# Performance work log

Measured on AMD Instinct MI355X. Metric: run time of the kernel, lower is better.

The kernel has to match this reference:

```python
import jax, jax.numpy as jnp
import numpy as np

N_NODES = 50000
NFEAT, NHID, NSSF, NCLASS = 512, 512, 256, 64
N_EDGES = 1600000
SP_RATE = 0.5
EPS = 1e-6


def spmm(src, dst, vals, m):
    # sparse [N,N] @ dense [N,F]: gather rows by src, scale, scatter-add to dst rows
    return jax.ops.segment_sum(m[src] * vals[:, None], dst, num_segments=N_NODES)


def setup_inputs() -> dict:
    key = jax.random.key(0)
    ks = jax.random.split(key, 12)
    stdv1 = 1.0 / np.sqrt(NFEAT)
    stdv2 = 1.0 / np.sqrt(NHID)
    inp = {
        "x": jax.random.normal(ks[0], (N_NODES, NFEAT), jnp.float32),
        "src": jax.random.randint(ks[1], (N_EDGES,), 0, N_NODES, jnp.int32),
        "dst": jax.random.randint(ks[2], (N_EDGES,), 0, N_NODES, jnp.int32),
        "vals": jax.random.uniform(ks[3], (N_EDGES,), jnp.float32),
        "W1": jax.random.uniform(ks[4], (NFEAT, NHID), jnp.float32, -stdv1, stdv1),
        "b1": jax.random.uniform(ks[5], (NHID,), jnp.float32, -stdv1, stdv1),
        "W2": jax.random.uniform(ks[6], (NHID, NHID), jnp.float32, -stdv2, stdv2),
        "b2": jax.random.uniform(ks[7], (NHID,), jnp.float32, -stdv2, stdv2),
        "W3": jax.random.uniform(ks[8], (NHID, NSSF), jnp.float32, -stdv2, stdv2),
        "b3": jax.random.uniform(ks[9], (NSSF,), jnp.float32, -stdv2, stdv2),
        "ssf": jax.random.normal(ks[10], (NSSF, NCLASS), jnp.float32) * 0.1,
        "sigma": jax.random.normal(ks[11], (), jnp.float32),
    }
    return inp


def reference(x, src, dst, vals, W1, b1, W2, b2, W3, b3, ssf, sigma):
    # 3 GCN layers: spmm(adj, x @ W + b)
    h = spmm(src, dst, vals, x @ W1 + b1)
    h = jax.nn.relu(h)
    h = spmm(src, dst, vals, h @ W2 + b2)
    h = jax.nn.relu(h)
    h = spmm(src, dst, vals, h @ W3 + b3)  # [N, NSSF]

    # sparsify subspace filter by magnitude threshold (static index)
    flat = jnp.abs(ssf).reshape(-1)
    filter_idx = round(NSSF * NCLASS * SP_RATE)
    threshold = jnp.sort(flat)[filter_idx]
    ssf_sp = jnp.where(jnp.abs(ssf) >= threshold, ssf, 0.0)

    out = h @ ssf_sp  # [N, NCLASS]

    # negative euclidean distance to each filter column: cdist(h, ssf_sp.T)
    sq = (jnp.sum(h * h, axis=1)[:, None]
          - 2.0 * out
          + jnp.sum(ssf_sp * ssf_sp, axis=0)[None, :])
    spatial_dist = -jnp.sqrt(jnp.maximum(sq, 1e-12))

    # cosine similarity of each row of h with each filter column
    hn = jnp.maximum(jnp.linalg.norm(h, axis=1), EPS)          # [N]
    cn = jnp.maximum(jnp.linalg.norm(ssf_sp, axis=0), EPS)     # [NCLASS]
    spatial_similarity = out / (hn[:, None] * cn[None, :])

    spatial_loss = 0.5 * (jax.nn.log_softmax(spatial_dist, axis=1)
                          + jax.nn.log_softmax(spatial_similarity, axis=1))
    return (out, ssf_sp, h, spatial_loss, sigma)
```

## Files before the change

kernel.cpp:

```cpp
#include <hip/hip_runtime.h>
#include <hip/hip_bf16.h>
#include <cstddef>

#define NN 50000
#define NE 1600000
#define NFEAT 512
#define NHID 512
#define NSSF 256
#define NCLASS 64
#define KTH 8193

typedef unsigned short u16;
typedef unsigned int u32;
typedef u16 u16x8 __attribute__((ext_vector_type(8)));
typedef u16 u16x4 __attribute__((ext_vector_type(4)));
typedef short bf16x8 __attribute__((ext_vector_type(8)));
typedef float f32x4 __attribute__((ext_vector_type(4)));

__device__ __forceinline__ float bf2f(u16 u) {
  union { unsigned u; float f; } c; c.u = ((unsigned)u) << 16; return c.f;
}
__device__ __forceinline__ u16 f2bf(float f) {
  __hip_bfloat16 b = __float2bfloat16(f);
  union { __hip_bfloat16 b; u16 u; } c; c.b = b; return c.u;
}

__device__ __forceinline__ void async_load16(const void* g, void* l) {
  __builtin_amdgcn_global_load_lds(
      (const __attribute__((address_space(1))) unsigned int*)g,
      (__attribute__((address_space(3))) unsigned int*)l, 16, 0, 0);
}

__global__ void k_hist(const int* __restrict__ dst, int* __restrict__ cnt) {
  int i = blockIdx.x * blockDim.x + threadIdx.x;
  int stride = gridDim.x * blockDim.x;
  for (; i < NE; i += stride) atomicAdd(&cnt[dst[i]], 1);
}

#define SCAN_B 196
__global__ void k_blksum(const int* __restrict__ cnt, int* __restrict__ bsum) {
  __shared__ int red[256];
  int b = blockIdx.x, t = threadIdx.x;
  int i = b * 256 + t;
  red[t] = (i < NN) ? cnt[i] : 0;
  __syncthreads();
  for (int s = 128; s > 0; s >>= 1) { if (t < s) red[t] += red[t + s]; __syncthreads(); }
  if (t == 0) bsum[b] = red[0];
}

__global__ void k_scanb(const int* __restrict__ bsum, int* __restrict__ boff,
                        int* __restrict__ rp) {
  __shared__ int buf[256];
  int t = threadIdx.x;
  int x = (t < SCAN_B) ? bsum[t] : 0;
  buf[t] = x;
  __syncthreads();
  for (int off = 1; off < 256; off <<= 1) {
    int y = (t >= off) ? buf[t - off] : 0;
    __syncthreads();
    buf[t] += y;
    __syncthreads();
  }
  if (t < SCAN_B) boff[t] = buf[t] - x;
  if (t == 0) rp[0] = 0;
}

__global__ void k_scanf(const int* __restrict__ cnt, const int* __restrict__ boff,
                        int* __restrict__ rp, int* __restrict__ fill) {
  __shared__ int buf[256];
  int b = blockIdx.x, t = threadIdx.x;
  int i = b * 256 + t;
  int x = (i < NN) ? cnt[i] : 0;
  buf[t] = x;
  __syncthreads();
  for (int off = 1; off < 256; off <<= 1) {
    int y = (t >= off) ? buf[t - off] : 0;
    __syncthreads();
    buf[t] += y;
    __syncthreads();
  }
  if (i < NN) {
    int incl = boff[b] + buf[t];
    rp[i + 1] = incl;
    fill[i] = incl - x;
  }
}

__global__ void k_scatter(const int* __restrict__ src, const int* __restrict__ dst,
                          const float* __restrict__ vals, int* __restrict__ fill,
                          u32* __restrict__ em) {
  int i = blockIdx.x * blockDim.x + threadIdx.x;
  int stride = gridDim.x * blockDim.x;
  for (; i < NE; i += stride) {
    int p = atomicAdd(&fill[dst[i]], 1);
    em[p] = (u32)src[i] | ((u32)f2bf(vals[i]) << 16);
  }
}

__global__ void k_cvt_bf16(const float* __restrict__ x, u16* __restrict__ xb, int n4) {
  int i = blockIdx.x * blockDim.x + threadIdx.x;
  if (i < n4) {
    float4 v = *(const float4*)(x + (size_t)i * 4);
    u16x4 o;
    o[0] = f2bf(v.x); o[1] = f2bf(v.y); o[2] = f2bf(v.z); o[3] = f2bf(v.w);
    *(u16x4*)(xb + (size_t)i * 4) = o;
  }
}

__global__ void k_wt(const float* __restrict__ W, u16* __restrict__ Wt, int K, int N) {
  int idx = blockIdx.x * blockDim.x + threadIdx.x;
  if (idx < N * K) {
    int n = idx / K, k = idx % K;
    Wt[idx] = f2bf(W[(size_t)k * N + n]);
  }
}

__global__ __launch_bounds__(256, 2) void k_gemm_mfma(
    const u16* __restrict__ A, const u16* __restrict__ Bt,
    const float* __restrict__ bias, u16* __restrict__ C,
    int M, int K, int N)
{
  __shared__ __align__(16) u16 As[128 * 32];
  __shared__ __align__(16) u16 Bs[128 * 32];
  int tid = threadIdx.x;
  int bm = blockIdx.y * 128;
  int bn = blockIdx.x * 128;
  int wave = tid >> 6, lane = tid & 63;

  int lrow = lane >> 2, lcol = (lane & 3) * 8;
  int arow0 = wave * 32 + lrow;
  int arow1 = wave * 32 + 16 + lrow;
  int garow0 = bm + arow0; if (garow0 >= M) garow0 = M - 1;
  int garow1 = bm + arow1; if (garow1 >= M) garow1 = M - 1;
  const u16* Ap0 = A + (size_t)garow0 * K + lcol;
  const u16* Ap1 = A + (size_t)garow1 * K + lcol;
  const u16* Bp0 = Bt + (size_t)(bn + arow0) * K + lcol;
  const u16* Bp1 = Bt + (size_t)(bn + arow1) * K + lcol;
  u16* lA0 = &As[(wave * 32) * 32];
  u16* lA1 = &As[(wave * 32 + 16) * 32];
  u16* lB0 = &Bs[(wave * 32) * 32];
  u16* lB1 = &Bs[(wave * 32 + 16) * 32];

  int wm = (wave >> 1) * 64, wn = (wave & 1) * 64;
  int m16 = lane & 15, quad = lane >> 4;

  f32x4 zz = {0.f, 0.f, 0.f, 0.f};
  f32x4 acc[4][4];
#pragma unroll
  for (int i = 0; i < 4; i++)
#pragma unroll
    for (int j = 0; j < 4; j++) acc[i][j] = zz;

  for (int k0 = 0; k0 < K; k0 += 32) {
    async_load16(Ap0 + k0, lA0);
    async_load16(Ap1 + k0, lA1);
    async_load16(Bp0 + k0, lB0);
    async_load16(Bp1 + k0, lB1);
    __syncthreads();

    bf16x8 af[4], bw[4];
#pragma unroll
    for (int i = 0; i < 4; i++)
      af[i] = *(const bf16x8*)&As[(wm + i * 16 + m16) * 32 + quad * 8];
#pragma unroll
    for (int j = 0; j < 4; j++)
      bw[j] = *(const bf16x8*)&Bs[(wn + j * 16 + m16) * 32 + quad * 8];
#pragma unroll
    for (int i = 0; i < 4; i++)
#pragma unroll
      for (int j = 0; j < 4; j++)
        acc[i][j] = __builtin_amdgcn_mfma_f32_16x16x32_bf16(af[i], bw[j], acc[i][j], 0, 0, 0);
    __syncthreads();
  }

#pragma unroll
  for (int j = 0; j < 4; j++) {
    int col = bn + wn + j * 16 + m16;
    float bv = bias[col];
#pragma unroll
    for (int i = 0; i < 4; i++) {
      int rbase = bm + wm + i * 16 + quad * 4;
#pragma unroll
      for (int r = 0; r < 4; r++) {
        int row = rbase + r;
        if (row < M) C[(size_t)row * N + col] = f2bf(acc[i][j][r] + bv);
      }
    }
  }
}

__global__ __launch_bounds__(256) void k_spmm512(
    const int* __restrict__ rp, const u32* __restrict__ em,
    const u16* __restrict__ Xb, u16* __restrict__ Hb)
{
  int wave = threadIdx.x >> 6, lane = threadIdx.x & 63;
  int r = blockIdx.x * 4 + wave;
  if (r >= NN) return;
  int e0 = rp[r], e1 = rp[r + 1];
  float acc0[8], acc1[8];
#pragma unroll
  for (int j = 0; j < 8; j++) { acc0[j] = 0.f; acc1[j] = 0.f; }
  const u16* Xl = Xb + lane * 8;
  int e = e0;
  for (; e + 2 <= e1; e += 2) {
    u32 m0 = em[e], m1 = em[e + 1];
    float v0 = __uint_as_float(m0 & 0xFFFF0000u);
    float v1 = __uint_as_float(m1 & 0xFFFF0000u);
    u16x8 x0 = *(const u16x8*)(Xl + (size_t)(m0 & 0xFFFFu) * 512);
    u16x8 x1 = *(const u16x8*)(Xl + (size_t)(m1 & 0xFFFFu) * 512);
#pragma unroll
    for (int j = 0; j < 8; j++) {
      acc0[j] += v0 * bf2f(x0[j]);
      acc1[j] += v1 * bf2f(x1[j]);
    }
  }
  if (e < e1) {
    u32 m0 = em[e];
    float v0 = __uint_as_float(m0 & 0xFFFF0000u);
    u16x8 x0 = *(const u16x8*)(Xl + (size_t)(m0 & 0xFFFFu) * 512);
#pragma unroll
    for (int j = 0; j < 8; j++) acc0[j] += v0 * bf2f(x0[j]);
  }
  u16x8 o;
#pragma unroll
  for (int j = 0; j < 8; j++) o[j] = f2bf(fmaxf(acc0[j] + acc1[j], 0.f));
  *(u16x8*)(Hb + (size_t)r * 512 + lane * 8) = o;
}

__global__ __launch_bounds__(256) void k_spmm256(
    const int* __restrict__ rp, const u32* __restrict__ em,
    const u16* __restrict__ Xb, float* __restrict__ Hf,
    u16* __restrict__ Hb3, float* __restrict__ hsq)
{
  int wave = threadIdx.x >> 6, lane = threadIdx.x & 63;
  int r = blockIdx.x * 4 + wave;
  if (r >= NN) return;
  int e0 = rp[r], e1 = rp[r + 1];
  float4 a0 = make_float4(0.f, 0.f, 0.f, 0.f);
  float4 a1 = make_float4(0.f, 0.f, 0.f, 0.f);
  const u16* Xl = Xb + lane * 4;
  int e = e0;
  for (; e + 2 <= e1; e += 2) {
    u32 m0 = em[e], m1 = em[e + 1];
    float v0 = __uint_as_float(m0 & 0xFFFF0000u);
    float v1 = __uint_as_float(m1 & 0xFFFF0000u);
    u16x4 x0 = *(const u16x4*)(Xl + (size_t)(m0 & 0xFFFFu) * 256);
    u16x4 x1 = *(const u16x4*)(Xl + (size_t)(m1 & 0xFFFFu) * 256);
    a0.x += v0 * bf2f(x0[0]); a0.y += v0 * bf2f(x0[1]);
    a0.z += v0 * bf2f(x0[2]); a0.w += v0 * bf2f(x0[3]);
    a1.x += v1 * bf2f(x1[0]); a1.y += v1 * bf2f(x1[1]);
    a1.z += v1 * bf2f(x1[2]); a1.w += v1 * bf2f(x1[3]);
  }
  if (e < e1) {
    u32 m0 = em[e];
    float v0 = __uint_as_float(m0 & 0xFFFF0000u);
    u16x4 x0 = *(const u16x4*)(Xl + (size_t)(m0 & 0xFFFFu) * 256);
    a0.x += v0 * bf2f(x0[0]); a0.y += v0 * bf2f(x0[1]);
    a0.z += v0 * bf2f(x0[2]); a0.w += v0 * bf2f(x0[3]);
  }
  float4 o;
  o.x = a0.x + a1.x; o.y = a0.y + a1.y; o.z = a0.z + a1.z; o.w = a0.w + a1.w;
  *(float4*)(Hf + (size_t)r * 256 + lane * 4) = o;
  u16x4 ob;
  ob[0] = f2bf(o.x); ob[1] = f2bf(o.y); ob[2] = f2bf(o.z); ob[3] = f2bf(o.w);
  *(u16x4*)(Hb3 + (size_t)r * 256 + lane * 4) = ob;
  float s = o.x * o.x + o.y * o.y + o.z * o.z + o.w * o.w;
#pragma unroll
  for (int m = 1; m < 64; m <<= 1) s += __shfl_xor(s, m);
  if (lane == 0) hsq[r] = s;
}

__global__ void k_ssf(const float* __restrict__ ssf, const float* __restrict__ sigma,
                      float* __restrict__ o_ssf, float* __restrict__ csq,
                      float* __restrict__ cnm, float* __restrict__ o_sig)
{
  __shared__ float sv[NSSF * NCLASS];
  __shared__ int red[256];
  int tid = threadIdx.x;
  for (int i = tid; i < NSSF * NCLASS; i += 256) sv[i] = ssf[i];
  __syncthreads();
  unsigned lo = 0u, hi = 0x7f800000u;
  while (lo < hi) {
    unsigned mid = lo + ((hi - lo) >> 1);
    int c = 0;
    for (int i = tid; i < NSSF * NCLASS; i += 256)
      c += ((__float_as_uint(sv[i]) & 0x7fffffffu) <= mid) ? 1 : 0;
    red[tid] = c;
    __syncthreads();
    for (int s = 128; s > 0; s >>= 1) {
      if (tid < s) red[tid] += red[tid + s];
      __syncthreads();
    }
    int total = red[0];
    __syncthreads();
    if (total >= KTH) hi = mid; else lo = mid + 1;
  }
  float t = __uint_as_float(lo);
  for (int i = tid; i < NSSF * NCLASS; i += 256) {
    float v = sv[i];
    v = (fabsf(v) >= t) ? v : 0.f;
    sv[i] = v;
    o_ssf[i] = v;
  }
  __syncthreads();
  if (tid < 64) {
    float s = 0.f;
    for (int k = 0; k < NSSF; k++) { float v = sv[k * NCLASS + tid]; s += v * v; }
    csq[tid] = s;
    cnm[tid] = fmaxf(sqrtf(s), 1e-6f);
  }
  if (tid == 0) o_sig[0] = sigma[0];
}

#define SSTR 264
__global__ __launch_bounds__(256) void k_epi(
    const u16* __restrict__ hb, const float* __restrict__ hsq,
    const float* __restrict__ ssf_sp, const float* __restrict__ colsq,
    const float* __restrict__ cn, float* __restrict__ outp,
    float* __restrict__ lossp)
{
  __shared__ __align__(16) u16 sT[64 * SSTR];
  int tid = threadIdx.x;
  for (int i = tid; i < NCLASS * NSSF; i += 256) {
    int n = i & 63, k = i >> 6;
    sT[n * SSTR + k] = f2bf(ssf_sp[i]);
  }
  __syncthreads();

  int wave = tid >> 6, lane = tid & 63;
  int m16 = lane & 15, quad = lane >> 4;
  int rb = blockIdx.x * 64 + wave * 16;

  int arow = rb + m16; if (arow >= NN) arow = NN - 1;
  const u16* hp = hb + (size_t)arow * NSSF + quad * 8;
  bf16x8 a8[8];
#pragma unroll
  for (int ks = 0; ks < 8; ks++) a8[ks] = *(const bf16x8*)(hp + ks * 32);

  f32x4 zz = {0.f, 0.f, 0.f, 0.f};
  f32x4 acc[4];
#pragma unroll
  for (int j = 0; j < 4; j++) acc[j] = zz;
#pragma unroll
  for (int j = 0; j < 4; j++) {
    const u16* bp = &sT[(j * 16 + m16) * SSTR + quad * 8];
#pragma unroll
    for (int ks = 0; ks < 8; ks++) {
      bf16x8 b8 = *(const bf16x8*)(bp + ks * 32);
      acc[j] = __builtin_amdgcn_mfma_f32_16x16x32_bf16(a8[ks], b8, acc[j], 0, 0, 0);
    }
  }

  float csql[4], cnl[4];
#pragma unroll
  for (int j = 0; j < 4; j++) {
    int c = j * 16 + m16;
    csql[j] = colsq[c];
    cnl[j] = cn[c];
  }

#pragma unroll
  for (int reg = 0; reg < 4; reg++) {
    int row = rb + quad * 4 + reg;
    bool ok = row < NN;
    int rowc = ok ? row : NN - 1;
    float hs = hsq[rowc];
    float hn = fmaxf(sqrtf(hs), 1e-6f);
    float d[4], sm[4];
    float m1 = -3.4e38f, m2 = -3.4e38f;
#pragma unroll
    for (int j = 0; j < 4; j++) {
      float o = acc[j][reg];
      float sq = hs - 2.f * o + csql[j];
      d[j] = -sqrtf(fmaxf(sq, 1e-12f));
      sm[j] = o / (hn * cnl[j]);
      m1 = fmaxf(m1, d[j]);
      m2 = fmaxf(m2, sm[j]);
    }
#pragma unroll
    for (int msk = 1; msk < 16; msk <<= 1) {
      m1 = fmaxf(m1, __shfl_xor(m1, msk));
      m2 = fmaxf(m2, __shfl_xor(m2, msk));
    }
    float s1 = 0.f, s2 = 0.f;
#pragma unroll
    for (int j = 0; j < 4; j++) {
      s1 += expf(d[j] - m1);
      s2 += expf(sm[j] - m2);
    }
#pragma unroll
    for (int msk = 1; msk < 16; msk <<= 1) {
      s1 += __shfl_xor(s1, msk);
      s2 += __shfl_xor(s2, msk);
    }
    float l1 = logf(s1), l2 = logf(s2);
    if (ok) {
#pragma unroll
      for (int j = 0; j < 4; j++) {
        int c = j * 16 + m16;
        outp[(size_t)row * NCLASS + c] = acc[j][reg];
        lossp[(size_t)row * NCLASS + c] =
            0.5f * ((d[j] - m1 - l1) + (sm[j] - m2 - l2));
      }
    }
  }
}

extern "C" void kernel_launch(void* const* d_in, const int* in_sizes, int n_in,
                              void* d_out, int out_size, void* d_ws, size_t ws_size,
                              hipStream_t stream)
{
  (void)in_sizes; (void)n_in; (void)out_size; (void)ws_size;
  const float* x    = (const float*)d_in[0];
  const int*   src  = (const int*)  d_in[1];
  const int*   dst  = (const int*)  d_in[2];
  const float* vals = (const float*)d_in[3];
  const float* W1 = (const float*)d_in[4];
  const float* b1 = (const float*)d_in[5];
  const float* W2 = (const float*)d_in[6];
  const float* b2 = (const float*)d_in[7];
  const float* W3 = (const float*)d_in[8];
  const float* b3 = (const float*)d_in[9];
  const float* ssf   = (const float*)d_in[10];
  const float* sigma = (const float*)d_in[11];

  float* outf   = (float*)d_out;
  float* o_out  = outf;
  float* o_ssf  = outf + (size_t)NN * NCLASS;
  float* o_h    = o_ssf + NSSF * NCLASS;
  float* o_loss = o_h + (size_t)NN * NSSF;
  float* o_sig  = o_loss + (size_t)NN * NCLASS;

  u16* Xb  = (u16*)d_ws;
  u16* Yb  = Xb + (size_t)NN * NFEAT;
  u16* Hb  = Yb + (size_t)NN * NHID;
  u16* W1t = Hb + (size_t)NN * NHID;
  u16* W2t = W1t + (size_t)NFEAT * NHID;
  u16* W3t = W2t + (size_t)NHID * NHID;
  int* cnt = (int*)(W3t + (size_t)NSSF * NHID);
  int* rp  = cnt + NN;
  u32* em  = (u32*)(rp + 50016);
  int* bsum = (int*)(em + NE);
  int* boff = bsum + 256;
  float* csq = (float*)(boff + 256);
  float* cnm = csq + 64;
  float* hsq = cnm + 64;

  hipMemsetAsync(cnt, 0, NN * sizeof(int), stream);
  k_hist<<<1024, 256, 0, stream>>>(dst, cnt);
  k_blksum<<<SCAN_B, 256, 0, stream>>>(cnt, bsum);
  k_scanb<<<1, 256, 0, stream>>>(bsum, boff, rp);
  k_scanf<<<SCAN_B, 256, 0, stream>>>(cnt, boff, rp, cnt);
  k_scatter<<<1024, 256, 0, stream>>>(src, dst, vals, cnt, em);

  k_cvt_bf16<<<(NN * NFEAT / 4 + 255) / 256, 256, 0, stream>>>(x, Xb, NN * NFEAT / 4);
  k_wt<<<(NFEAT * NHID + 255) / 256, 256, 0, stream>>>(W1, W1t, NFEAT, NHID);
  k_wt<<<(NHID * NHID + 255) / 256, 256, 0, stream>>>(W2, W2t, NHID, NHID);
  k_wt<<<(NHID * NSSF + 255) / 256, 256, 0, stream>>>(W3, W3t, NHID, NSSF);

  k_gemm_mfma<<<dim3(4, 391), 256, 0, stream>>>(Xb, W1t, b1, Yb, NN, NFEAT, NHID);
  k_spmm512<<<NN / 4, 256, 0, stream>>>(rp, em, Yb, Hb);
  k_gemm_mfma<<<dim3(4, 391), 256, 0, stream>>>(Hb, W2t, b2, Yb, NN, NHID, NHID);
  k_spmm512<<<NN / 4, 256, 0, stream>>>(rp, em, Yb, Xb);
  k_gemm_mfma<<<dim3(2, 391), 256, 0, stream>>>(Xb, W3t, b3, Yb, NN, NHID, NSSF);
  k_spmm256<<<NN / 4, 256, 0, stream>>>(rp, em, Yb, o_h, Hb, hsq);

  k_ssf<<<1, 256, 0, stream>>>(ssf, sigma, o_ssf, csq, cnm, o_sig);
  k_epi<<<(NN + 63) / 64, 256, 0, stream>>>(Hb, hsq, o_ssf, csq, cnm, o_out, o_loss);
}
```

Before: 1.175 ms.

## Fuse fp32-to-bf16 conversion into first GEMM, merge weight transposes, unroll SpMM

The first GEMM now reads fp32 x directly and converts it to bf16 while staging into padded shared memory. This removes the separate conversion kernel and its 50 MB bf16 write plus re-read. The three weight-transpose launches are merged into one kernel, and the 512-wide SpMM loop is unrolled to four edges per iteration to keep more gathers in flight. The trade-off is that the first GEMM does synchronous fp32 global loads instead of async bf16 loads, which doubles A-side traffic per tile and may hurt overlap.

New measurement: 1.169 ms. Within noise of the previous version (-0.5%).

```diff
diff --git a/kernel.cpp b/kernel.cpp
--- a/kernel.cpp
+++ b/kernel.cpp
@@ -97,21 +97,108 @@
   }
 }
 
-__global__ void k_cvt_bf16(const float* __restrict__ x, u16* __restrict__ xb, int n4) {
-  int i = blockIdx.x * blockDim.x + threadIdx.x;
-  if (i < n4) {
-    float4 v = *(const float4*)(x + (size_t)i * 4);
-    u16x4 o;
-    o[0] = f2bf(v.x); o[1] = f2bf(v.y); o[2] = f2bf(v.z); o[3] = f2bf(v.w);
-    *(u16x4*)(xb + (size_t)i * 4) = o;
-  }
-}
-
-__global__ void k_wt(const float* __restrict__ W, u16* __restrict__ Wt, int K, int N) {
+__global__ void k_wt_all(const float* __restrict__ W1, const float* __restrict__ W2,
+                         const float* __restrict__ W3, u16* __restrict__ W1t,
+                         u16* __restrict__ W2t, u16* __restrict__ W3t) {
   int idx = blockIdx.x * blockDim.x + threadIdx.x;
-  if (idx < N * K) {
-    int n = idx / K, k = idx % K;
-    Wt[idx] = f2bf(W[(size_t)k * N + n]);
+  const int S1 = NFEAT * NHID;
+  const int S2 = S1 + NHID * NHID;
+  const int S3 = S2 + NHID * NSSF;
+  if (idx < S1) {
+    int n = idx >> 9, k = idx & 511;
+    W1t[idx] = f2bf(W1[(size_t)k * NHID + n]);
+  } else if (idx < S2) {
+    int j = idx - S1;
+    int n = j >> 9, k = j & 511;
+    W2t[j] = f2bf(W2[(size_t)k * NHID + n]);
+  } else if (idx < S3) {
+    int j = idx - S2;
+    int n = j >> 9, k = j & 511;
+    W3t[j] = f2bf(W3[(size_t)k * NSSF + n]);
+  }
+}
+
+__global__ __launch_bounds__(256, 2) void k_gemm_f32a(
+    const float* __restrict__ A, const u16* __restrict__ Bt,
+    const float* __restrict__ bias, u16* __restrict__ C,
+    int M, int K, int N)
+{
+  __shared__ __align__(16) u16 As[128 * 40];
+  __shared__ __align__(16) u16 Bs[128 * 32];
+  int tid = threadIdx.x;
+  int bm = blockIdx.y * 128;
+  int bn = blockIdx.x * 128;
+  int wave = tid >> 6, lane = tid & 63;
+
+  int arows[4], acol4[4];
+  const float* Aps[4];
+#pragma unroll
+  for (int i = 0; i < 4; i++) {
+    int f = tid + i * 256;
+    int row = f >> 3, c4 = (f & 7) * 4;
+    arows[i] = row; acol4[i] = c4;
+    int gr = bm + row; if (gr >= M) gr = M - 1;
+    Aps[i] = A + (size_t)gr * K + c4;
+  }
+  int lrow = lane >> 2, lcol = (lane & 3) * 8;
+  const u16* Bp0 = Bt + (size_t)(bn + wave * 32 + lrow) * K + lcol;
+  const u16* Bp1 = Bt + (size_t)(bn + wave * 32 + 16 + lrow) * K + lcol;
+  u16* lB0 = &Bs[(wave * 32) * 32];
+  u16* lB1 = &Bs[(wave * 32 + 16) * 32];
+
+  int wm = (wave >> 1) * 64, wn = (wave & 1) * 64;
+  int m16 = lane & 15, quad = lane >> 4;
+
+  f32x4 zz = {0.f, 0.f, 0.f, 0.f};
+  f32x4 acc[4][4];
+#pragma unroll
+  for (int i = 0; i < 4; i++)
+#pragma unroll
+    for (int j = 0; j < 4; j++) acc[i][j] = zz;
+
+  for (int k0 = 0; k0 < K; k0 += 32) {
+    async_load16(Bp0 + k0, lB0);
+    async_load16(Bp1 + k0, lB1);
+    float4 av[4];
+#pragma unroll
+    for (int i = 0; i < 4; i++) av[i] = *(const float4*)(Aps[i] + k0);
+#pragma unroll
+    for (int i = 0; i < 4; i++) {
+      u16x4 o;
+      o[0] = f2bf(av[i].x); o[1] = f2bf(av[i].y);
+      o[2] = f2bf(av[i].z); o[3] = f2bf(av[i].w);
+      *(u16x4*)&As[arows[i] * 40 + acol4[i]] = o;
+    }
+    __syncthreads();
+
+    bf16x8 af[4], bw[4];
+#pragma unroll
+    for (int i = 0; i < 4; i++)
+      af[i] = *(const bf16x8*)&As[(wm + i * 16 + m16) * 40 + quad * 8];
+#pragma unroll
+    for (int j = 0; j < 4; j++)
+      bw[j] = *(const bf16x8*)&Bs[(wn + j * 16 + m16) * 32 + quad * 8];
+#pragma unroll
+    for (int i = 0; i < 4; i++)
+#pragma unroll
+      for (int j = 0; j < 4; j++)
+        acc[i][j] = __builtin_amdgcn_mfma_f32_16x16x32_bf16(af[i], bw[j], acc[i][j], 0, 0, 0);
+    __syncthreads();
+  }
+
+#pragma unroll
+  for (int j = 0; j < 4; j++) {
+    int col = bn + wn + j * 16 + m16;
+    float bv = bias[col];
+#pragma unroll
+    for (int i = 0; i < 4; i++) {
+      int rbase = bm + wm + i * 16 + quad * 4;
+#pragma unroll
+      for (int r = 0; r < 4; r++) {
+        int row = rbase + r;
+        if (row < M) C[(size_t)row * N + col] = f2bf(acc[i][j][r] + bv);
+      }
+    }
   }
 }
 
@@ -202,19 +289,25 @@
   for (int j = 0; j < 8; j++) { acc0[j] = 0.f; acc1[j] = 0.f; }
   const u16* Xl = Xb + lane * 8;
   int e = e0;
-  for (; e + 2 <= e1; e += 2) {
-    u32 m0 = em[e], m1 = em[e + 1];
+  for (; e + 4 <= e1; e += 4) {
+    u32 m0 = em[e], m1 = em[e + 1], m2 = em[e + 2], m3 = em[e + 3];
     float v0 = __uint_as_float(m0 & 0xFFFF0000u);
     float v1 = __uint_as_float(m1 & 0xFFFF0000u);
+    float v2 = __uint_as_float(m2 & 0xFFFF0000u);
+    float v3 = __uint_as_float(m3 & 0xFFFF0000u);
     u16x8 x0 = *(const u16x8*)(Xl + (size_t)(m0 & 0xFFFFu) * 512);
     u16x8 x1 = *(const u16x8*)(Xl + (size_t)(m1 & 0xFFFFu) * 512);
+    u16x8 x2 = *(const u16x8*)(Xl + (size_t)(m2 & 0xFFFFu) * 512);
+    u16x8 x3 = *(const u16x8*)(Xl + (size_t)(m3 & 0xFFFFu) * 512);
 #pragma unroll
     for (int j = 0; j < 8; j++) {
       acc0[j] += v0 * bf2f(x0[j]);
       acc1[j] += v1 * bf2f(x1[j]);
-    }
-  }
-  if (e < e1) {
+      acc0[j] += v2 * bf2f(x2[j]);
+      acc1[j] += v3 * bf2f(x3[j]);
+    }
+  }
+  for (; e < e1; ++e) {
     u32 m0 = em[e];
     float v0 = __uint_as_float(m0 & 0xFFFF0000u);
     u16x8 x0 = *(const u16x8*)(Xl + (size_t)(m0 & 0xFFFFu) * 512);
@@ -453,12 +546,10 @@
   k_scanf<<<SCAN_B, 256, 0, stream>>>(cnt, boff, rp, cnt);
   k_scatter<<<1024, 256, 0, stream>>>(src, dst, vals, cnt, em);
 
-  k_cvt_bf16<<<(NN * NFEAT / 4 + 255) / 256, 256, 0, stream>>>(x, Xb, NN * NFEAT / 4);
-  k_wt<<<(NFEAT * NHID + 255) / 256, 256, 0, stream>>>(W1, W1t, NFEAT, NHID);
-  k_wt<<<(NHID * NHID + 255) / 256, 256, 0, stream>>>(W2, W2t, NHID, NHID);
-  k_wt<<<(NHID * NSSF + 255) / 256, 256, 0, stream>>>(W3, W3t, NHID, NSSF);
-
-  k_gemm_mfma<<<dim3(4, 391), 256, 0, stream>>>(Xb, W1t, b1, Yb, NN, NFEAT, NHID);
+  k_wt_all<<<(NFEAT * NHID * 2 + NHID * NSSF + 255) / 256, 256, 0, stream>>>(
+      W1, W2, W3, W1t, W2t, W3t);
+
+  k_gemm_f32a<<<dim3(4, 391), 256, 0, stream>>>(x, W1t, b1, Yb, NN, NFEAT, NHID);
   k_spmm512<<<NN / 4, 256, 0, stream>>>(rp, em, Yb, Hb);
   k_gemm_mfma<<<dim3(4, 391), 256, 0, stream>>>(Hb, W2t, b2, Yb, NN, NHID, NHID);
   k_spmm512<<<NN / 4, 256, 0, stream>>>(rp, em, Yb, Xb);
```
